# Kernel tuning notes

Hardware: AMD Instinct MI355X
Metric: run time of the kernel (lower is better)

## Reference

```python
import jax, jax.numpy as jnp
import numpy as np

B, S, I, H = 256, 512, 512, 1024


def setup_inputs() -> dict:
    key = jax.random.key(0)
    ks = jax.random.split(key, 7)
    s = 1.0 / np.sqrt(H)
    x = jax.random.normal(ks[0], (B, S, I), jnp.float32)
    # equinox GRUCell params: weight_ih (3H,I), weight_hh (3H,H), bias (3H,), bias_n (H,)
    wi = jax.random.uniform(ks[1], (3 * H, I), jnp.float32, -s, s)
    wh = jax.random.uniform(ks[2], (3 * H, H), jnp.float32, -s, s)
    bi = jax.random.uniform(ks[3], (3 * H,), jnp.float32, -s, s)
    bn = jax.random.uniform(ks[4], (H,), jnp.float32, -s, s)
    # final Linear(H, 1)
    sl = 1.0 / np.sqrt(H)
    wl = jax.random.uniform(ks[5], (1, H), jnp.float32, -sl, sl)
    bl = jax.random.uniform(ks[6], (1,), jnp.float32, -sl, sl)
    return {"x": x, "wi": wi, "wh": wh, "bi": bi, "bn": bn, "wl": wl, "bl": bl}


def reference(x, wi, wh, bi, bn, wl, bl):
    # x: (B, S, I). Precompute input-side gate projections for all timesteps
    # (same math as per-step wi @ x_t + bi, hoisted out of the scan).
    ig_all = jnp.einsum('bsi,gi->sbg', x, wi) + bi  # (S, B, 3H)

    def step(h, ig_t):
        hg = h @ wh.T  # (B, 3H)
        ir, iz, ia = jnp.split(ig_t, 3, axis=-1)
        hr, hz, ha = jnp.split(hg, 3, axis=-1)
        r = jax.nn.sigmoid(ir + hr)          # reset gate
        z = jax.nn.sigmoid(iz + hz)          # update gate (equinox 'inp')
        n = jnp.tanh(ia + r * (ha + bn))     # candidate (uses bias_n)
        h_new = n + z * (h - n)              # equinox GRUCell output
        return h_new, None

    h0 = jnp.zeros((x.shape[0], wh.shape[1]), x.dtype)
    hT, _ = jax.lax.scan(step, h0, ig_all)
    energies = hT @ wl.T + bl  # (B, 1)
    return jnp.squeeze(energies, axis=-1)  # (B,)
```

## Files before the change

kernel.cpp:

```cpp
#include <hip/hip_runtime.h>
#include <hip/hip_bf16.h>


#define B_  256
#define S_  512
#define I_  512
#define H_  1024

typedef __bf16 bf16x8 __attribute__((ext_vector_type(8)));
typedef float  f32x4  __attribute__((ext_vector_type(4)));
typedef float  f32x4v __attribute__((ext_vector_type(4)));

union U16x8 { int4 i; bf16x8 b; unsigned short s[8]; unsigned u[4]; };

__device__ __forceinline__ unsigned pack2bf(float lo, float hi) {
    union { float f; unsigned u; } a, b;
    a.f = lo; b.f = hi;
    return __builtin_amdgcn_perm(b.u + 0x8000u, a.u + 0x8000u, 0x07060302u);
}
__device__ __forceinline__ bf16x8 ldb(const unsigned short* p) {
    U16x8 u; u.i = *(const int4*)p; return u.b;
}
__device__ __forceinline__ bf16x8 ldh_dev(const unsigned long long* p) {
    unsigned long long lo = __hip_atomic_load(p,     __ATOMIC_RELAXED, __HIP_MEMORY_SCOPE_AGENT);
    unsigned long long hi = __hip_atomic_load(p + 1, __ATOMIC_RELAXED, __HIP_MEMORY_SCOPE_AGENT);
    union { unsigned long long q[2]; bf16x8 b; } u;
    u.q[0] = lo; u.q[1] = hi; return u.b;
}

__global__ void prep_kernel(const float* __restrict__ wh, const float* __restrict__ wi,
                            const float* __restrict__ x,
                            unsigned* __restrict__ hbA_u, unsigned* __restrict__ whb_u,
                            unsigned* __restrict__ wib_u, unsigned* __restrict__ flags,
                            unsigned* __restrict__ xb_u) {
    int idx = blockIdx.x * blockDim.x + threadIdx.x;
    int stride = gridDim.x * blockDim.x;
    const float2* wh2 = (const float2*)wh;
    const float2* wi2 = (const float2*)wi;
    for (int i = idx; i < 3 * H_ * H_ / 2; i += stride) { float2 v = wh2[i]; whb_u[i] = pack2bf(v.x, v.y); }
    for (int i = idx; i < 3 * H_ * I_ / 2; i += stride) { float2 v = wi2[i]; wib_u[i] = pack2bf(v.x, v.y); }
    for (int i = idx; i < B_ * H_ / 2; i += stride) hbA_u[i] = 0u;
    if (idx < 256 * 4 * 16) flags[idx] = 0u;
    if (xb_u) {
        const float2* x2 = (const float2*)x;
        const int n = B_ * S_ * I_ / 2;
        for (int i = idx; i < n; i += stride) { float2 v = x2[i]; xb_u[i] = pack2bf(v.x, v.y); }
    }
}

template<int XB>
__global__ __launch_bounds__(256, 1) void gru_persistent(
    const float* __restrict__ x,
    const unsigned short* __restrict__ xbp,
    const unsigned short* __restrict__ whb,
    const unsigned short* __restrict__ wib,
    const float* __restrict__ bi,
    const float* __restrict__ bn,
    unsigned short* __restrict__ hbufA,
    unsigned short* __restrict__ hbufB,
    float* __restrict__ h32g,
    unsigned* __restrict__ flags)
{
    __shared__ float partial[4 * 3 * 16 * 68];
    __shared__ float h32s[64 * 17];

    const int tid  = threadIdx.x;
    const int w    = tid >> 6;
    const int lane = tid & 63;
    const int col  = lane & 15;
    const int quad = lane >> 4;

    const int hblk = blockIdx.x & 63;
    const int mt   = blockIdx.x >> 6;
    const int k0   = hblk << 4;
    const int b0   = mt << 6;
    const int kwh  = w << 8;
    const int kwi  = w << 7;

    bf16x8 Bh[3][8];
    bf16x8 Bx[3][4];
    #pragma unroll
    for (int g = 0; g < 3; ++g) {
        const unsigned short* bh = whb + ((size_t)(g * H_ + k0 + col)) * H_ + kwh + (quad << 3);
        #pragma unroll
        for (int kk = 0; kk < 8; ++kk) Bh[g][kk] = ldb(bh + kk * 32);
        const unsigned short* bx = wib + ((size_t)(g * H_ + k0 + col)) * I_ + kwi + (quad << 3);
        #pragma unroll
        for (int kk = 0; kk < 4; ++kk) Bx[g][kk] = ldb(bx + kk * 32);
    }

    const int hcol = k0 + col;
    const float bir = bi[hcol], biz = bi[H_ + hcol], bia = bi[2 * H_ + hcol], bnv = bn[hcol];

    for (int i = tid; i < 64 * 17; i += 256) h32s[i] = 0.f;
    __syncthreads();

    unsigned* myflag = flags + (((blockIdx.x << 2) + w) << 4);
    const unsigned* spin_fp = flags +
        ((((mt << 6) + (w << 4) + (lane >> 2)) * 4 + (lane & 3)) << 4);

    const f32x4 zero4 = {0.f, 0.f, 0.f, 0.f};

    for (int t = 0; t < S_; ++t) {
        f32x4 acc[4][4];
        #pragma unroll
        for (int mi = 0; mi < 4; ++mi)
            #pragma unroll
            for (int j = 0; j < 4; ++j) acc[mi][j] = zero4;

        if constexpr (XB) {
            const unsigned short* xbase = xbp + ((size_t)(b0 + col) * S_ + (size_t)t) * I_ + kwi + (quad << 3);
            #pragma unroll
            for (int kk = 0; kk < 4; ++kk) {
                #pragma unroll
                for (int mi = 0; mi < 4; ++mi) {
                    bf16x8 a = ldb(xbase + (size_t)mi * 16 * S_ * I_ + kk * 32);
                    acc[mi][0] = __builtin_amdgcn_mfma_f32_16x16x32_bf16(a, Bx[0][kk], acc[mi][0], 0, 0, 0);
                    acc[mi][1] = __builtin_amdgcn_mfma_f32_16x16x32_bf16(a, Bx[1][kk], acc[mi][1], 0, 0, 0);
                    acc[mi][2] = __builtin_amdgcn_mfma_f32_16x16x32_bf16(a, Bx[2][kk], acc[mi][2], 0, 0, 0);
                }
            }
        } else {
            const float* xbase = x + ((size_t)(b0 + col) * S_ + (size_t)t) * I_ + kwi + (quad << 3);
            #pragma unroll
            for (int kk = 0; kk < 4; ++kk) {
                #pragma unroll
                for (int mi = 0; mi < 4; ++mi) {
                    const float* p = xbase + (size_t)mi * 16 * S_ * I_ + kk * 32;
                    f32x4v f0 = __builtin_nontemporal_load((const f32x4v*)p);
                    f32x4v f1 = __builtin_nontemporal_load((const f32x4v*)(p + 4));
                    U16x8 u;
                    u.u[0] = pack2bf(f0[0], f0[1]);
                    u.u[1] = pack2bf(f0[2], f0[3]);
                    u.u[2] = pack2bf(f1[0], f1[1]);
                    u.u[3] = pack2bf(f1[2], f1[3]);
                    bf16x8 a = u.b;
                    acc[mi][0] = __builtin_amdgcn_mfma_f32_16x16x32_bf16(a, Bx[0][kk], acc[mi][0], 0, 0, 0);
                    acc[mi][1] = __builtin_amdgcn_mfma_f32_16x16x32_bf16(a, Bx[1][kk], acc[mi][1], 0, 0, 0);
                    acc[mi][2] = __builtin_amdgcn_mfma_f32_16x16x32_bf16(a, Bx[2][kk], acc[mi][2], 0, 0, 0);
                }
            }
        }

        if (t > 0) {
            while (__hip_atomic_load(spin_fp, __ATOMIC_RELAXED, __HIP_MEMORY_SCOPE_AGENT) < (unsigned)t)
                __builtin_amdgcn_s_sleep(1);
            asm volatile("" ::: "memory");
        }

        const unsigned short* hcur = (t & 1) ? hbufB : hbufA;
        const unsigned short* hrow = hcur + (size_t)(b0 + col) * H_ + kwh + (quad << 3);
        {
            bf16x8 hf[2][4];
            #pragma unroll
            for (int mi = 0; mi < 4; ++mi)
                hf[0][mi] = ldh_dev((const unsigned long long*)(hrow + (size_t)mi * 16 * H_));
            #pragma unroll
            for (int kk = 0; kk < 8; ++kk) {
                if (kk < 7) {
                    #pragma unroll
                    for (int mi = 0; mi < 4; ++mi)
                        hf[(kk + 1) & 1][mi] = ldh_dev((const unsigned long long*)(hrow + (size_t)mi * 16 * H_ + (kk + 1) * 32));
                }
                #pragma unroll
                for (int mi = 0; mi < 4; ++mi) {
                    bf16x8 a = hf[kk & 1][mi];
                    acc[mi][0] = __builtin_amdgcn_mfma_f32_16x16x32_bf16(a, Bh[0][kk], acc[mi][0], 0, 0, 0);
                    acc[mi][1] = __builtin_amdgcn_mfma_f32_16x16x32_bf16(a, Bh[1][kk], acc[mi][1], 0, 0, 0);
                    acc[mi][3] = __builtin_amdgcn_mfma_f32_16x16x32_bf16(a, Bh[2][kk], acc[mi][3], 0, 0, 0);
                }
            }
        }

        #pragma unroll
        for (int mi = 0; mi < 4; ++mi) {
            if (mi == w) continue;
            int slot = mi - (mi > w ? 1 : 0);
            float* dst = partial + (size_t)((w * 3 + slot) * 16) * 68;
            #pragma unroll
            for (int j = 0; j < 4; ++j)
                #pragma unroll
                for (int r = 0; r < 4; ++r)
                    dst[((quad << 2) + r) * 68 + j * 16 + col] = acc[mi][j][r];
        }
        __syncthreads();

        #pragma unroll
        for (int r = 0; r < 4; ++r) {
            float sr = 0.f, sz = 0.f, sia = 0.f, sha = 0.f;
            #pragma unroll
            for (int mi = 0; mi < 4; ++mi)
                if (mi == w) { sr = acc[mi][0][r]; sz = acc[mi][1][r]; sia = acc[mi][2][r]; sha = acc[mi][3][r]; }
            #pragma unroll
            for (int p = 0; p < 4; ++p) {
                if (p == w) continue;
                int slot = w - (w > p ? 1 : 0);
                const float* src = partial + (size_t)(((p * 3 + slot) * 16 + (quad << 2) + r)) * 68 + col;
                sr  += src[0];
                sz  += src[16];
                sia += src[32];
                sha += src[48];
            }
            float rg = 1.f / (1.f + __expf(-(sr + bir)));
            float zg = 1.f / (1.f + __expf(-(sz + biz)));
            float pa = sia + bia + rg * (sha + bnv);
            float e2 = __expf(2.f * pa);
            float ng = 1.f - 2.f / (e2 + 1.f);
            int m = (w << 4) + (quad << 2) + r;
            float hold = h32s[m * 17 + col];
            float hnew = ng + zg * (hold - ng);
            h32s[m * 17 + col] = hnew;
            if (t == S_ - 1) h32g[(size_t)(b0 + m) * H_ + k0 + col] = hnew;
        }
        __syncthreads();

        {
            unsigned short* hnext = (t & 1) ? hbufA : hbufB;
            const int pm = (w << 4) + (lane >> 2);
            const int pc = (lane & 3) << 2;
            const float* hp = h32s + pm * 17 + pc;
            unsigned long long pkt = (unsigned long long)pack2bf(hp[0], hp[1])
                                   | ((unsigned long long)pack2bf(hp[2], hp[3]) << 32);
            __hip_atomic_store((unsigned long long*)(hnext + (size_t)(b0 + pm) * H_ + k0 + pc),
                               pkt, __ATOMIC_RELAXED, __HIP_MEMORY_SCOPE_AGENT);
            asm volatile("s_waitcnt vmcnt(0)" ::: "memory");
            if (lane == 0)
                __hip_atomic_store(myflag, (unsigned)(t + 1), __ATOMIC_RELAXED, __HIP_MEMORY_SCOPE_AGENT);
        }
    }
}

__global__ __launch_bounds__(256) void final_kernel(const float* __restrict__ h32,
                                                    const float* __restrict__ wl,
                                                    const float* __restrict__ bl,
                                                    float* __restrict__ out) {
    const int b = blockIdx.x;
    float s = 0.f;
    for (int k = threadIdx.x; k < H_; k += 256)
        s += h32[((size_t)b << 10) + k] * wl[k];
    #pragma unroll
    for (int off = 32; off > 0; off >>= 1)
        s += __shfl_down(s, off, 64);
    __shared__ float red[4];
    const int wave = threadIdx.x >> 6;
    const int lane = threadIdx.x & 63;
    if (lane == 0) red[wave] = s;
    __syncthreads();
    if (threadIdx.x == 0)
        out[b] = red[0] + red[1] + red[2] + red[3] + bl[0];
}

extern "C" void kernel_launch(void* const* d_in, const int* in_sizes, int n_in,
                              void* d_out, int out_size, void* d_ws, size_t ws_size,
                              hipStream_t stream) {
    const float* x  = (const float*)d_in[0];
    const float* wi = (const float*)d_in[1];
    const float* wh = (const float*)d_in[2];
    const float* bi = (const float*)d_in[3];
    const float* bn = (const float*)d_in[4];
    const float* wl = (const float*)d_in[5];
    const float* bl = (const float*)d_in[6];
    float* out = (float*)d_out;

    char* ws = (char*)d_ws;
    float*          h32g  = (float*)ws;
    unsigned short* hbA   = (unsigned short*)(ws + (1u << 20));
    unsigned short* hbB   = (unsigned short*)(ws + (1u << 20) + (512u << 10));
    unsigned short* whb   = (unsigned short*)(ws + (2u << 20));
    unsigned short* wib   = (unsigned short*)(ws + (8u << 20));
    unsigned*       flags = (unsigned*)(ws + (11u << 20));
    const bool use_xb = ws_size >= (140ull << 20);
    unsigned short* xbw = use_xb ? (unsigned short*)(ws + (12ull << 20)) : nullptr;

    prep_kernel<<<1024, 256, 0, stream>>>(wh, wi, x, (unsigned*)hbA, (unsigned*)whb,
                                          (unsigned*)wib, flags, (unsigned*)xbw);
    if (use_xb)
        gru_persistent<1><<<256, 256, 0, stream>>>(x, xbw, whb, wib, bi, bn, hbA, hbB, h32g, flags);
    else
        gru_persistent<0><<<256, 256, 0, stream>>>(x, nullptr, whb, wib, bi, bn, hbA, hbB, h32g, flags);
    final_kernel<<<B_, 256, 0, stream>>>(h32g, wl, bl, out);
}
```

Before: 7.889 ms.

## Add ring-buffered bf16 x prefetch mode for mid-size workspaces

Adds a third mode that holds a small ring of bf16-converted x timesteps in the workspace. Each block converts one future timestep slice while the recurrence runs, so mid-size workspaces no longer fall back to loading fp32 x and converting it on every step. It also samples the step flag early, before the x-projection MFMAs, so the spin loop can be skipped when the flag is already set. The ring correctness depends on the barrier ordering of the step flags. The full-precompute path now needs a slightly larger workspace threshold (141 MB instead of 140 MB).

```diff
diff --git a/kernel.cpp b/kernel.cpp
--- a/kernel.cpp
+++ b/kernel.cpp
@@ -32,7 +32,8 @@
                             const float* __restrict__ x,
                             unsigned* __restrict__ hbA_u, unsigned* __restrict__ whb_u,
                             unsigned* __restrict__ wib_u, unsigned* __restrict__ flags,
-                            unsigned* __restrict__ xb_u) {
+                            unsigned* __restrict__ xb_u, unsigned* __restrict__ xw_u,
+                            int W) {
     int idx = blockIdx.x * blockDim.x + threadIdx.x;
     int stride = gridDim.x * blockDim.x;
     const float2* wh2 = (const float2*)wh;
@@ -46,12 +47,26 @@
         const int n = B_ * S_ * I_ / 2;
         for (int i = idx; i < n; i += stride) { float2 v = x2[i]; xb_u[i] = pack2bf(v.x, v.y); }
     }
-}
-
-template<int XB>
+    if (xw_u) {
+        const int total = 4 * W * 16384;
+        for (int i = idx; i < total; i += stride) {
+            int gslot = i >> 14;
+            int rest  = i & 16383;
+            int row   = rest >> 8;
+            int cp    = rest & 255;
+            int mt    = gslot / W;
+            int s     = gslot - mt * W;
+            const float2 v = *(const float2*)(x + ((size_t)(mt * 64 + row) * S_ + s) * I_ + (cp << 1));
+            xw_u[i] = pack2bf(v.x, v.y);
+        }
+    }
+}
+
+template<int MODE>
 __global__ __launch_bounds__(256, 1) void gru_persistent(
     const float* __restrict__ x,
     const unsigned short* __restrict__ xbp,
+    unsigned* __restrict__ xww,
     const unsigned short* __restrict__ whb,
     const unsigned short* __restrict__ wib,
     const float* __restrict__ bi,
@@ -59,7 +74,8 @@
     unsigned short* __restrict__ hbufA,
     unsigned short* __restrict__ hbufB,
     float* __restrict__ h32g,
-    unsigned* __restrict__ flags)
+    unsigned* __restrict__ flags,
+    int wmask)
 {
     __shared__ float partial[4 * 3 * 16 * 68];
     __shared__ float h32s[64 * 17];
@@ -108,13 +124,31 @@
             #pragma unroll
             for (int j = 0; j < 4; ++j) acc[mi][j] = zero4;
 
-        if constexpr (XB) {
+        bool early_ok = true;
+        if (t > 0)
+            early_ok = (__hip_atomic_load(spin_fp, __ATOMIC_RELAXED, __HIP_MEMORY_SCOPE_AGENT) >= (unsigned)t);
+
+        if constexpr (MODE == 2) {
             const unsigned short* xbase = xbp + ((size_t)(b0 + col) * S_ + (size_t)t) * I_ + kwi + (quad << 3);
             #pragma unroll
             for (int kk = 0; kk < 4; ++kk) {
                 #pragma unroll
                 for (int mi = 0; mi < 4; ++mi) {
                     bf16x8 a = ldb(xbase + (size_t)mi * 16 * S_ * I_ + kk * 32);
+                    acc[mi][0] = __builtin_amdgcn_mfma_f32_16x16x32_bf16(a, Bx[0][kk], acc[mi][0], 0, 0, 0);
+                    acc[mi][1] = __builtin_amdgcn_mfma_f32_16x16x32_bf16(a, Bx[1][kk], acc[mi][1], 0, 0, 0);
+                    acc[mi][2] = __builtin_amdgcn_mfma_f32_16x16x32_bf16(a, Bx[2][kk], acc[mi][2], 0, 0, 0);
+                }
+            }
+        } else if constexpr (MODE == 1) {
+            const int W = wmask + 1;
+            const unsigned short* xbase = xbp
+                + ((size_t)((mt * W + (t & wmask)) * 64 + col)) * I_ + kwi + (quad << 3);
+            #pragma unroll
+            for (int kk = 0; kk < 4; ++kk) {
+                #pragma unroll
+                for (int mi = 0; mi < 4; ++mi) {
+                    bf16x8 a = ldh_dev((const unsigned long long*)(xbase + (size_t)mi * 16 * I_ + kk * 32));
                     acc[mi][0] = __builtin_amdgcn_mfma_f32_16x16x32_bf16(a, Bx[0][kk], acc[mi][0], 0, 0, 0);
                     acc[mi][1] = __builtin_amdgcn_mfma_f32_16x16x32_bf16(a, Bx[1][kk], acc[mi][1], 0, 0, 0);
                     acc[mi][2] = __builtin_amdgcn_mfma_f32_16x16x32_bf16(a, Bx[2][kk], acc[mi][2], 0, 0, 0);
@@ -143,8 +177,10 @@
         }
 
         if (t > 0) {
-            while (__hip_atomic_load(spin_fp, __ATOMIC_RELAXED, __HIP_MEMORY_SCOPE_AGENT) < (unsigned)t)
-                __builtin_amdgcn_s_sleep(1);
+            if (!early_ok) {
+                while (__hip_atomic_load(spin_fp, __ATOMIC_RELAXED, __HIP_MEMORY_SCOPE_AGENT) < (unsigned)t)
+                    __builtin_amdgcn_s_sleep(1);
+            }
             asm volatile("" ::: "memory");
         }
 
@@ -169,6 +205,20 @@
                     acc[mi][1] = __builtin_amdgcn_mfma_f32_16x16x32_bf16(a, Bh[1][kk], acc[mi][1], 0, 0, 0);
                     acc[mi][3] = __builtin_amdgcn_mfma_f32_16x16x32_bf16(a, Bh[2][kk], acc[mi][3], 0, 0, 0);
                 }
+            }
+        }
+
+        if constexpr (MODE == 1) {
+            const int W = wmask + 1;
+            const int s = t + W - 1;
+            if (t >= 1 && s < S_) {
+                const int flat = (hblk << 8) + tid;
+                const int row  = flat >> 8;
+                const int cp   = flat & 255;
+                const float2 v = *(const float2*)(x + ((size_t)(b0 + row) * S_ + s) * I_ + (cp << 1));
+                const unsigned pkt = pack2bf(v.x, v.y);
+                __hip_atomic_store(xww + ((size_t)((mt * W + (s & wmask))) << 14) + flat,
+                                   pkt, __ATOMIC_RELAXED, __HIP_MEMORY_SCOPE_AGENT);
             }
         }
 
@@ -269,14 +319,29 @@
     unsigned short* whb   = (unsigned short*)(ws + (2u << 20));
     unsigned short* wib   = (unsigned short*)(ws + (8u << 20));
     unsigned*       flags = (unsigned*)(ws + (11u << 20));
-    const bool use_xb = ws_size >= (140ull << 20);
-    unsigned short* xbw = use_xb ? (unsigned short*)(ws + (12ull << 20)) : nullptr;
+
+    unsigned short* xbw = nullptr;
+    unsigned*       xww = nullptr;
+    int W = 0;
+    if (ws_size >= (141ull << 20)) {
+        xbw = (unsigned short*)(ws + (12ull << 20));
+    } else if (ws_size >= (13ull << 20)) {
+        size_t avail = ws_size - (12ull << 20);
+        W = 4;
+        while (W < 64 && ((size_t)(W * 2) << 18) <= avail) W <<= 1;
+        xww = (unsigned*)(ws + (12ull << 20));
+    }
 
     prep_kernel<<<1024, 256, 0, stream>>>(wh, wi, x, (unsigned*)hbA, (unsigned*)whb,
-                                          (unsigned*)wib, flags, (unsigned*)xbw);
-    if (use_xb)
-        gru_persistent<1><<<256, 256, 0, stream>>>(x, xbw, whb, wib, bi, bn, hbA, hbB, h32g, flags);
+                                          (unsigned*)wib, flags, (unsigned*)xbw, xww, W);
+    if (xbw)
+        gru_persistent<2><<<256, 256, 0, stream>>>(x, xbw, nullptr, whb, wib, bi, bn,
+                                                   hbA, hbB, h32g, flags, 0);
+    else if (xww)
+        gru_persistent<1><<<256, 256, 0, stream>>>(x, (const unsigned short*)xww, xww, whb, wib, bi, bn,
+                                                   hbA, hbB, h32g, flags, W - 1);
     else
-        gru_persistent<0><<<256, 256, 0, stream>>>(x, nullptr, whb, wib, bi, bn, hbA, hbB, h32g, flags);
+        gru_persistent<0><<<256, 256, 0, stream>>>(x, nullptr, nullptr, whb, wib, bi, bn,
+                                                   hbA, hbB, h32g, flags, 0);
     final_kernel<<<B_, 256, 0, stream>>>(h32g, wl, bl, out);
 }
```

New measurement: 8.220 ms. 4.2% more time.
